# Optimization experiments

Hardware: AMD Instinct MI355X
Metric: run time of the kernel (lower is better)

The kernel has to match this reference:

```python
import jax, jax.numpy as jnp
from jax import lax
import numpy as np

VOCAB = 50000
EMBED = 300
UNITS = 512          # num_nodes[0]
D1 = 1024            # num_nodes[1]
D2 = 1024            # num_nodes[2]
NUM_CLASSES = 20
B, T = 64, 512


def setup_inputs() -> dict:
    key = jax.random.key(0)
    ks = jax.random.split(key, 12)
    s = 0.02
    return {
        "tokens": jax.random.randint(ks[0], (B, T), 0, VOCAB),
        "emb": jax.random.normal(ks[1], (VOCAB, EMBED), jnp.float32) * s,
        "Wx": jax.random.normal(ks[2], (EMBED, 4 * UNITS), jnp.float32) * s,
        "Wh": jax.random.normal(ks[3], (UNITS, 4 * UNITS), jnp.float32) * s,
        "b": jnp.zeros((4 * UNITS,), jnp.float32),
        "W1": jax.random.normal(ks[4], (UNITS, D1), jnp.float32) * s,
        "b1": jnp.zeros((D1,), jnp.float32),
        "W2": jax.random.normal(ks[5], (D1, D2), jnp.float32) * s,
        "b2": jnp.zeros((D2,), jnp.float32),
        "Wo": jax.random.normal(ks[6], (D2, NUM_CLASSES), jnp.float32) * s,
        "bo": jnp.zeros((NUM_CLASSES,), jnp.float32),
    }


def reference(tokens, emb, Wx, Wh, b, W1, b1, W2, b2, Wo, bo):
    # Embedding with mask_zero=True: token 0 timesteps are masked -> LSTM skips
    # the state update (Keras semantics).
    mask = (tokens != 0)                               # [B, T]
    x = emb[tokens]                                    # [B, T, E]
    units = Wh.shape[0]
    # Precompute input contribution to the gates (parallel over time).
    xg = jnp.einsum('bte,eg->btg', x, Wx) + b          # [B, T, 4U]

    def step(carry, inp):
        h, c = carry
        g_x, m = inp                                   # [B,4U], [B]
        g = g_x + h @ Wh                               # [B, 4U]
        i, f, cc, o = jnp.split(g, 4, axis=-1)         # Keras gate order i,f,c,o
        i = jax.nn.sigmoid(i)
        f = jax.nn.sigmoid(f)
        o = jax.nn.sigmoid(o)
        # activation='relu' replaces tanh in candidate and output transform.
        c_new = f * c + i * jax.nn.relu(cc)
        h_new = o * jax.nn.relu(c_new)
        m = m[:, None]
        h = jnp.where(m, h_new, h)
        c = jnp.where(m, c_new, c)
        return (h, c), None

    h0 = jnp.zeros((tokens.shape[0], units), x.dtype)
    (h, _), _ = lax.scan(step, (h0, h0),
                         (jnp.swapaxes(xg, 0, 1), mask.T))  # scan over T

    h = jax.nn.relu(h @ W1 + b1)
    h = jax.nn.relu(h @ W2 + b2)
    return jax.nn.softmax(h @ Wo + bo)
```

## Files before the change

### kernel.cpp

```cpp
#include <hip/hip_runtime.h>
#include <hip/hip_bf16.h>

#define B_   64
#define T_   512
#define E_   300
#define U_   512
#define G4_  2048
#define D1_  1024
#define D2_  1024
#define NC_  20
#define KP_  320

typedef __bf16 bf16x8 __attribute__((ext_vector_type(8)));
typedef float  f32x4  __attribute__((ext_vector_type(4)));

__device__ __forceinline__ float sigmoidf_(float x) { return 1.0f / (1.0f + __expf(-x)); }

__device__ __forceinline__ void gl_lds16(const void* g, void* l) {
    __builtin_amdgcn_global_load_lds(
        (const __attribute__((address_space(1))) unsigned int*)g,
        (__attribute__((address_space(3))) unsigned int*)l, 16, 0, 0);
}

__global__ void init_kernel(unsigned int* __restrict__ hz, int* __restrict__ flags) {
    int idx = blockIdx.x * 256 + threadIdx.x;
    if (idx < (B_ * U_ / 2)) hz[idx] = 0u;
    if (idx < 256) flags[idx] = 0;
}

__global__ __launch_bounds__(256) void prep_wxT(const float* __restrict__ Wx,
                                                __hip_bfloat16* __restrict__ wxT) {
    __shared__ __hip_bfloat16 t[64][65];
    const int n0 = blockIdx.x * 64;
    const int k0 = blockIdx.y * 64;
    const int tid = threadIdx.x;
    for (int i = tid; i < 4096; i += 256) {
        int r = i >> 6, c = i & 63;
        int k = k0 + r;
        float v = (k < E_) ? Wx[(size_t)k * G4_ + n0 + c] : 0.f;
        t[r][c] = __float2bfloat16(v);
    }
    __syncthreads();
    for (int i = tid; i < 4096; i += 256) {
        int r = i >> 6, c = i & 63;
        wxT[(size_t)(n0 + r) * KP_ + k0 + c] = t[c][r];
    }
}

__global__ __launch_bounds__(256) void prep_xb(const int* __restrict__ tokens,
                                               const float* __restrict__ emb,
                                               __hip_bfloat16* __restrict__ xb) {
    const int row = blockIdx.x * 4 + (threadIdx.x >> 6);
    const int ln  = threadIdx.x & 63;
    const int tok = tokens[row];
    const float* src = emb + (size_t)tok * E_;
    __hip_bfloat16* dst = xb + (size_t)row * KP_;
    for (int k = ln; k < KP_; k += 64)
        dst[k] = (k < E_) ? __float2bfloat16(src[k]) : __float2bfloat16(0.f);
}

__global__ __launch_bounds__(256) void xg_gemm(const __hip_bfloat16* __restrict__ xb,
                                               const __hip_bfloat16* __restrict__ wxT,
                                               const float* __restrict__ bias,
                                               __hip_bfloat16* __restrict__ xg) {
    const int n0g = blockIdx.x * 128;
    const int bt0 = blockIdx.y * 128;
    const int tid = threadIdx.x;
    const int w   = tid >> 6;
    const int ln  = tid & 63;
    const int fn  = ln & 15;
    const int quad = ln >> 4;
    const int m0  = (w >> 1) * 64;
    const int n0w = (w & 1) * 64;

    __shared__ __align__(16) __hip_bfloat16 As[128 * 32];
    __shared__ __align__(16) __hip_bfloat16 Bs[128 * 32];

    f32x4 acc[4][4];
    #pragma unroll
    for (int im = 0; im < 4; ++im)
        #pragma unroll
        for (int in = 0; in < 4; ++in)
            acc[im][in] = (f32x4){0.f, 0.f, 0.f, 0.f};

    const __hip_bfloat16* ga = xb  + (size_t)(bt0 + w * 32 + (ln >> 2)) * KP_ + (ln & 3) * 8;
    const __hip_bfloat16* gb = wxT + (size_t)(n0g + w * 32 + (ln >> 2)) * KP_ + (ln & 3) * 8;

    for (int kt = 0; kt < KP_ / 32; ++kt) {
        gl_lds16(ga,             &As[(w * 32) * 32]);
        gl_lds16(ga + 16 * KP_,  &As[(w * 32 + 16) * 32]);
        gl_lds16(gb,             &Bs[(w * 32) * 32]);
        gl_lds16(gb + 16 * KP_,  &Bs[(w * 32 + 16) * 32]);
        ga += 32; gb += 32;
        __syncthreads();

        bf16x8 af[4], bf[4];
        #pragma unroll
        for (int im = 0; im < 4; ++im)
            af[im] = *(const bf16x8*)&As[(m0 + im * 16 + fn) * 32 + quad * 8];
        #pragma unroll
        for (int in = 0; in < 4; ++in)
            bf[in] = *(const bf16x8*)&Bs[(n0w + in * 16 + fn) * 32 + quad * 8];
        #pragma unroll
        for (int im = 0; im < 4; ++im)
            #pragma unroll
            for (int in = 0; in < 4; ++in)
                acc[im][in] = __builtin_amdgcn_mfma_f32_16x16x32_bf16(
                    af[im], bf[in], acc[im][in], 0, 0, 0);
        __syncthreads();
    }

    #pragma unroll
    for (int in = 0; in < 4; ++in) {
        const int n = n0g + n0w + in * 16 + fn;
        const float bv = bias[n];
        #pragma unroll
        for (int im = 0; im < 4; ++im) {
            #pragma unroll
            for (int r = 0; r < 4; ++r) {
                int m = bt0 + m0 + im * 16 + quad * 4 + r;
                int bb = m >> 9, tt = m & 511;
                xg[(size_t)(tt * B_ + bb) * G4_ + n] =
                    __float2bfloat16(acc[im][in][r] + bv);
            }
        }
    }
}

__global__ __launch_bounds__(256) void lstm_kernel(const __hip_bfloat16* __restrict__ xg,
                                                   const int* __restrict__ tokens,
                                                   const float* __restrict__ Wh,
                                                   __hip_bfloat16* __restrict__ hbuf,
                                                   int* __restrict__ flags) {
    const int tid  = threadIdx.x;
    const int lane = tid & 63;
    const int wave = tid >> 6;
    const int x  = blockIdx.x & 7;
    const int r_ = blockIdx.x >> 3;
    const int ub = x * 4 + (r_ & 3);
    const int g  = r_ >> 2;
    const int u0 = ub * 16;

    __shared__ __align__(16) __hip_bfloat16 whsT[64][520];
    __shared__ __align__(16) __hip_bfloat16 hs[16][520];
    __shared__ float gbuf[16][64];
    __shared__ unsigned mask_lds[16][16];

    for (int idx = tid; idx < 64 * 512; idx += 256) {
        int c = idx & 63, k = idx >> 6;
        int col = ((c >> 4) << 9) + u0 + (c & 15);
        whsT[c][k] = __float2bfloat16(Wh[(size_t)k * G4_ + col]);
    }
    {
        int m = tid >> 4, wi = tid & 15;
        const int4* tp = (const int4*)(tokens + (size_t)(g * 16 + m) * T_ + wi * 32);
        unsigned bits = 0;
        #pragma unroll
        for (int q = 0; q < 8; ++q) {
            int4 v = tp[q];
            bits |= (v.x != 0 ? 1u : 0u) << (q * 4 + 0);
            bits |= (v.y != 0 ? 1u : 0u) << (q * 4 + 1);
            bits |= (v.z != 0 ? 1u : 0u) << (q * 4 + 2);
            bits |= (v.w != 0 ? 1u : 0u) << (q * 4 + 3);
        }
        mask_lds[m][wi] = bits;
    }

    float c0 = 0.f, c1 = 0.f, h0 = 0.f, h1 = 0.f;
    int* gflags = flags + g * 64;

    const int fn   = lane & 15;
    const int quad = lane >> 4;
    const int fc   = wave * 16 + fn;
    const int fcol = ((fc >> 4) << 9) + u0 + (fc & 15);

    __syncthreads();

    for (int s = 0; s < T_; ++s) {
        float xv[4];
        {
            #pragma unroll
            for (int r = 0; r < 4; ++r)
                xv[r] = __bfloat162float(
                    xg[(size_t)(s * B_ + g * 16 + quad * 4 + r) * G4_ + fcol]);
        }

        if (s > 0) {
            if (tid < 32) {
                while (__hip_atomic_load(&gflags[tid], __ATOMIC_RELAXED,
                                         __HIP_MEMORY_SCOPE_AGENT) < s)
                    __builtin_amdgcn_s_sleep(2);
            }
            __syncthreads();
        }

        {
            const uint4* hp = (const uint4*)(hbuf + (size_t)((s & 1) * B_ + g * 16) * U_);
            uint4 t0, t1, t2, t3;
            asm volatile(
                "global_load_dwordx4 %0, %4, off sc0 sc1\n\t"
                "global_load_dwordx4 %1, %5, off sc0 sc1\n\t"
                "global_load_dwordx4 %2, %6, off sc0 sc1\n\t"
                "s_waitcnt vmcnt(0)\n\t"
                "global_load_dwordx4 %3, %7, off sc0 sc1\n\t"
                "s_waitcnt vmcnt(0)"
                : "=&v"(t0), "=&v"(t1), "=&v"(t2), "=&v"(t3)
                : "v"(hp + tid), "v"(hp + tid + 256), "v"(hp + tid + 512),
                  "v"(hp + tid + 768)
                : "memory");
            int i0 = tid;        *((uint4*)&hs[i0 >> 6][(i0 & 63) * 8]) = t0;
            int i1 = tid + 256;  *((uint4*)&hs[i1 >> 6][(i1 & 63) * 8]) = t1;
            int i2 = tid + 512;  *((uint4*)&hs[i2 >> 6][(i2 & 63) * 8]) = t2;
            int i3 = tid + 768;  *((uint4*)&hs[i3 >> 6][(i3 & 63) * 8]) = t3;
        }
        __syncthreads();

        {
            f32x4 acc;
            #pragma unroll
            for (int r = 0; r < 4; ++r) acc[r] = xv[r];
            const __hip_bfloat16* arow = &hs[fn][quad * 8];
            const __hip_bfloat16* brow = &whsT[fc][quad * 8];
            #pragma unroll
            for (int kk = 0; kk < 16; ++kk) {
                bf16x8 av = *(const bf16x8*)(arow + kk * 32);
                bf16x8 bv = *(const bf16x8*)(brow + kk * 32);
                acc = __builtin_amdgcn_mfma_f32_16x16x32_bf16(av, bv, acc, 0, 0, 0);
            }
            #pragma unroll
            for (int r = 0; r < 4; ++r)
                gbuf[quad * 4 + r][fc] = acc[r];
        }
        __syncthreads();

        if (tid < 128) {
            const int m  = tid >> 3;
            const int u2 = (tid & 7) << 1;
            float gi0 = sigmoidf_(gbuf[m][u2]),       gi1 = sigmoidf_(gbuf[m][u2 + 1]);
            float gf0 = sigmoidf_(gbuf[m][16 + u2]),  gf1 = sigmoidf_(gbuf[m][17 + u2]);
            float gc0 = gbuf[m][32 + u2],             gc1 = gbuf[m][33 + u2];
            float go0 = sigmoidf_(gbuf[m][48 + u2]),  go1 = sigmoidf_(gbuf[m][49 + u2]);
            float cn0 = gf0 * c0 + gi0 * fmaxf(gc0, 0.f);
            float cn1 = gf1 * c1 + gi1 * fmaxf(gc1, 0.f);
            float hn0 = go0 * fmaxf(cn0, 0.f);
            float hn1 = go1 * fmaxf(cn1, 0.f);
            if ((mask_lds[m][s >> 5] >> (s & 31)) & 1u) {
                c0 = cn0; c1 = cn1; h0 = hn0; h1 = hn1;
            }
            __hip_bfloat162 hv;
            hv.x = __float2bfloat16(h0);
            hv.y = __float2bfloat16(h1);
            unsigned wv;
            __builtin_memcpy(&wv, &hv, 4);
            unsigned* dst = (unsigned*)hbuf +
                (((((s + 1) & 1) * B_ + g * 16 + m) * U_ + u0 + u2) >> 1);
            __hip_atomic_store(dst, wv, __ATOMIC_RELAXED, __HIP_MEMORY_SCOPE_AGENT);
        }
        __syncthreads();
        if (tid == 0)
            __hip_atomic_store(&gflags[ub], s + 1, __ATOMIC_RELAXED,
                               __HIP_MEMORY_SCOPE_AGENT);
    }
}

__global__ __launch_bounds__(256) void fc1_kernel(const __hip_bfloat16* __restrict__ h,
                                                  const float* __restrict__ W,
                                                  const float* __restrict__ bias,
                                                  float* __restrict__ y) {
    int b = blockIdx.x >> 2, ch = blockIdx.x & 3;
    __shared__ float xrow[U_];
    for (int i = threadIdx.x; i < U_; i += 256)
        xrow[i] = __bfloat162float(h[b * U_ + i]);
    __syncthreads();
    int n = ch * 256 + threadIdx.x;
    float acc = 0.f;
    #pragma unroll 4
    for (int k = 0; k < U_; ++k) acc = fmaf(xrow[k], W[(size_t)k * D1_ + n], acc);
    y[b * D1_ + n] = fmaxf(acc + bias[n], 0.f);
}

__global__ __launch_bounds__(256) void fc2_kernel(const float* __restrict__ x,
                                                  const float* __restrict__ W,
                                                  const float* __restrict__ bias,
                                                  float* __restrict__ y) {
    int b = blockIdx.x >> 2, ch = blockIdx.x & 3;
    __shared__ float xrow[D1_];
    for (int i = threadIdx.x; i < D1_; i += 256) xrow[i] = x[b * D1_ + i];
    __syncthreads();
    int n = ch * 256 + threadIdx.x;
    float acc = 0.f;
    #pragma unroll 4
    for (int k = 0; k < D1_; ++k) acc = fmaf(xrow[k], W[(size_t)k * D2_ + n], acc);
    y[b * D2_ + n] = fmaxf(acc + bias[n], 0.f);
}

__global__ __launch_bounds__(64) void out_kernel(const float* __restrict__ h2,
                                                 const float* __restrict__ Wo,
                                                 const float* __restrict__ bo,
                                                 float* __restrict__ out) {
    int b = blockIdx.x;
    __shared__ float xrow[D2_];
    __shared__ float lg[NC_];
    __shared__ float red[2];
    for (int i = threadIdx.x; i < D2_; i += 64) xrow[i] = h2[b * D2_ + i];
    __syncthreads();
    if (threadIdx.x < NC_) {
        float a = bo[threadIdx.x];
        for (int k = 0; k < D2_; ++k) a = fmaf(xrow[k], Wo[k * NC_ + threadIdx.x], a);
        lg[threadIdx.x] = a;
    }
    __syncthreads();
    if (threadIdx.x == 0) {
        float mx = lg[0];
        for (int c = 1; c < NC_; ++c) mx = fmaxf(mx, lg[c]);
        float sm = 0.f;
        for (int c = 0; c < NC_; ++c) sm += expf(lg[c] - mx);
        red[0] = mx; red[1] = 1.0f / sm;
    }
    __syncthreads();
    if (threadIdx.x < NC_)
        out[b * NC_ + threadIdx.x] = expf(lg[threadIdx.x] - red[0]) * red[1];
}

extern "C" void kernel_launch(void* const* d_in, const int* in_sizes, int n_in,
                              void* d_out, int out_size, void* d_ws, size_t ws_size,
                              hipStream_t stream) {
    const int*   tokens = (const int*)d_in[0];
    const float* emb    = (const float*)d_in[1];
    const float* Wx     = (const float*)d_in[2];
    const float* Wh     = (const float*)d_in[3];
    const float* b      = (const float*)d_in[4];
    const float* W1     = (const float*)d_in[5];
    const float* b1     = (const float*)d_in[6];
    const float* W2     = (const float*)d_in[7];
    const float* b2     = (const float*)d_in[8];
    const float* Wo     = (const float*)d_in[9];
    const float* bo     = (const float*)d_in[10];
    float* out = (float*)d_out;

    char* ws = (char*)d_ws;
    const size_t XG_BYTES   = (size_t)T_ * B_ * G4_ * 2;
    const size_t HBUF_BYTES = (size_t)2 * B_ * U_ * 2;
    __hip_bfloat16* xg   = (__hip_bfloat16*)ws;
    __hip_bfloat16* hbuf = (__hip_bfloat16*)(ws + XG_BYTES);
    int* flags           = (int*)(ws + XG_BYTES + HBUF_BYTES);
    char* p = ws + XG_BYTES + HBUF_BYTES + 1024;
    float* h1            = (float*)p;                 p += (size_t)B_ * D1_ * 4;
    float* h2            = (float*)p;                 p += (size_t)B_ * D2_ * 4;
    __hip_bfloat16* xb   = (__hip_bfloat16*)p;        p += (size_t)B_ * T_ * KP_ * 2;
    __hip_bfloat16* wxT  = (__hip_bfloat16*)p;

    init_kernel<<<64, 256, 0, stream>>>((unsigned int*)hbuf, flags);
    prep_wxT<<<dim3(32, 5), 256, 0, stream>>>(Wx, wxT);
    prep_xb<<<(B_ * T_) / 4, 256, 0, stream>>>(tokens, emb, xb);
    xg_gemm<<<dim3(16, 256), 256, 0, stream>>>(xb, wxT, b, xg);
    lstm_kernel<<<128, 256, 0, stream>>>(xg, tokens, Wh, hbuf, flags);
    fc1_kernel<<<256, 256, 0, stream>>>(hbuf, W1, b1, h1);
    fc2_kernel<<<256, 256, 0, stream>>>(h1, W2, b2, h2);
    out_kernel<<<64, 64, 0, stream>>>(h2, Wo, bo, out);
}
```

Baseline: 1.693 ms.

## Interleave two batch groups per LSTM block to overlap sync latency

Each LSTM block now handles two 16-row batch groups instead of one, halving the grid to 64 blocks. The step loop alternates between the groups, so the flag wait and hidden-state load for group B overlap with the gate compute for group A, hiding cross-block synchronisation latency. It also drops an intermediate s_waitcnt so all four hidden-state loads are issued together. In exchange each block does twice the MFMA and elementwise work per step serially and holds more LDS, and the group A flag is now published later in the step.

```diff
diff --git a/kernel.cpp b/kernel.cpp
--- a/kernel.cpp
+++ b/kernel.cpp
@@ -138,13 +138,15 @@
     const int x  = blockIdx.x & 7;
     const int r_ = blockIdx.x >> 3;
     const int ub = x * 4 + (r_ & 3);
-    const int g  = r_ >> 2;
+    const int p  = r_ >> 2;
+    const int gA = p * 2;
+    const int gB = p * 2 + 1;
     const int u0 = ub * 16;
 
     __shared__ __align__(16) __hip_bfloat16 whsT[64][520];
-    __shared__ __align__(16) __hip_bfloat16 hs[16][520];
-    __shared__ float gbuf[16][64];
-    __shared__ unsigned mask_lds[16][16];
+    __shared__ __align__(16) __hip_bfloat16 hs[2][16][520];
+    __shared__ float gbuf[2][16][64];
+    __shared__ unsigned mask_lds[2][16][16];
 
     for (int idx = tid; idx < 64 * 512; idx += 256) {
         int c = idx & 63, k = idx >> 6;
@@ -153,21 +155,27 @@
     }
     {
         int m = tid >> 4, wi = tid & 15;
-        const int4* tp = (const int4*)(tokens + (size_t)(g * 16 + m) * T_ + wi * 32);
-        unsigned bits = 0;
-        #pragma unroll
-        for (int q = 0; q < 8; ++q) {
-            int4 v = tp[q];
-            bits |= (v.x != 0 ? 1u : 0u) << (q * 4 + 0);
-            bits |= (v.y != 0 ? 1u : 0u) << (q * 4 + 1);
-            bits |= (v.z != 0 ? 1u : 0u) << (q * 4 + 2);
-            bits |= (v.w != 0 ? 1u : 0u) << (q * 4 + 3);
-        }
-        mask_lds[m][wi] = bits;
-    }
-
-    float c0 = 0.f, c1 = 0.f, h0 = 0.f, h1 = 0.f;
-    int* gflags = flags + g * 64;
+        #pragma unroll
+        for (int grp = 0; grp < 2; ++grp) {
+            const int4* tp = (const int4*)(tokens +
+                (size_t)((p * 2 + grp) * 16 + m) * T_ + wi * 32);
+            unsigned bits = 0;
+            #pragma unroll
+            for (int q = 0; q < 8; ++q) {
+                int4 v = tp[q];
+                bits |= (v.x != 0 ? 1u : 0u) << (q * 4 + 0);
+                bits |= (v.y != 0 ? 1u : 0u) << (q * 4 + 1);
+                bits |= (v.z != 0 ? 1u : 0u) << (q * 4 + 2);
+                bits |= (v.w != 0 ? 1u : 0u) << (q * 4 + 3);
+            }
+            mask_lds[grp][m][wi] = bits;
+        }
+    }
+
+    float cA0 = 0.f, cA1 = 0.f, hA0 = 0.f, hA1 = 0.f;
+    float cB0 = 0.f, cB1 = 0.f, hB0 = 0.f, hB1 = 0.f;
+    int* gfA = flags + gA * 64;
+    int* gfB = flags + gB * 64;
 
     const int fn   = lane & 15;
     const int quad = lane >> 4;
@@ -177,49 +185,47 @@
     __syncthreads();
 
     for (int s = 0; s < T_; ++s) {
-        float xv[4];
-        {
-            #pragma unroll
-            for (int r = 0; r < 4; ++r)
-                xv[r] = __bfloat162float(
-                    xg[(size_t)(s * B_ + g * 16 + quad * 4 + r) * G4_ + fcol]);
+        float xvA[4], xvB[4];
+        #pragma unroll
+        for (int r = 0; r < 4; ++r) {
+            xvA[r] = __bfloat162float(
+                xg[(size_t)(s * B_ + gA * 16 + quad * 4 + r) * G4_ + fcol]);
+            xvB[r] = __bfloat162float(
+                xg[(size_t)(s * B_ + gB * 16 + quad * 4 + r) * G4_ + fcol]);
         }
 
         if (s > 0) {
             if (tid < 32) {
-                while (__hip_atomic_load(&gflags[tid], __ATOMIC_RELAXED,
+                while (__hip_atomic_load(&gfA[tid], __ATOMIC_RELAXED,
                                          __HIP_MEMORY_SCOPE_AGENT) < s)
                     __builtin_amdgcn_s_sleep(2);
             }
             __syncthreads();
         }
-
         {
-            const uint4* hp = (const uint4*)(hbuf + (size_t)((s & 1) * B_ + g * 16) * U_);
+            const uint4* hp = (const uint4*)(hbuf + (size_t)((s & 1) * B_ + gA * 16) * U_);
             uint4 t0, t1, t2, t3;
             asm volatile(
                 "global_load_dwordx4 %0, %4, off sc0 sc1\n\t"
                 "global_load_dwordx4 %1, %5, off sc0 sc1\n\t"
                 "global_load_dwordx4 %2, %6, off sc0 sc1\n\t"
-                "s_waitcnt vmcnt(0)\n\t"
                 "global_load_dwordx4 %3, %7, off sc0 sc1\n\t"
                 "s_waitcnt vmcnt(0)"
                 : "=&v"(t0), "=&v"(t1), "=&v"(t2), "=&v"(t3)
                 : "v"(hp + tid), "v"(hp + tid + 256), "v"(hp + tid + 512),
                   "v"(hp + tid + 768)
                 : "memory");
-            int i0 = tid;        *((uint4*)&hs[i0 >> 6][(i0 & 63) * 8]) = t0;
-            int i1 = tid + 256;  *((uint4*)&hs[i1 >> 6][(i1 & 63) * 8]) = t1;
-            int i2 = tid + 512;  *((uint4*)&hs[i2 >> 6][(i2 & 63) * 8]) = t2;
-            int i3 = tid + 768;  *((uint4*)&hs[i3 >> 6][(i3 & 63) * 8]) = t3;
-        }
-        __syncthreads();
-
+            int i0 = tid;        *((uint4*)&hs[0][i0 >> 6][(i0 & 63) * 8]) = t0;
+            int i1 = tid + 256;  *((uint4*)&hs[0][i1 >> 6][(i1 & 63) * 8]) = t1;
+            int i2 = tid + 512;  *((uint4*)&hs[0][i2 >> 6][(i2 & 63) * 8]) = t2;
+            int i3 = tid + 768;  *((uint4*)&hs[0][i3 >> 6][(i3 & 63) * 8]) = t3;
+        }
+        __syncthreads();
         {
             f32x4 acc;
             #pragma unroll
-            for (int r = 0; r < 4; ++r) acc[r] = xv[r];
-            const __hip_bfloat16* arow = &hs[fn][quad * 8];
+            for (int r = 0; r < 4; ++r) acc[r] = xvA[r];
+            const __hip_bfloat16* arow = &hs[0][fn][quad * 8];
             const __hip_bfloat16* brow = &whsT[fc][quad * 8];
             #pragma unroll
             for (int kk = 0; kk < 16; ++kk) {
@@ -229,36 +235,106 @@
             }
             #pragma unroll
             for (int r = 0; r < 4; ++r)
-                gbuf[quad * 4 + r][fc] = acc[r];
-        }
-        __syncthreads();
-
+                gbuf[0][quad * 4 + r][fc] = acc[r];
+        }
+        __syncthreads();
         if (tid < 128) {
             const int m  = tid >> 3;
             const int u2 = (tid & 7) << 1;
-            float gi0 = sigmoidf_(gbuf[m][u2]),       gi1 = sigmoidf_(gbuf[m][u2 + 1]);
-            float gf0 = sigmoidf_(gbuf[m][16 + u2]),  gf1 = sigmoidf_(gbuf[m][17 + u2]);
-            float gc0 = gbuf[m][32 + u2],             gc1 = gbuf[m][33 + u2];
-            float go0 = sigmoidf_(gbuf[m][48 + u2]),  go1 = sigmoidf_(gbuf[m][49 + u2]);
-            float cn0 = gf0 * c0 + gi0 * fmaxf(gc0, 0.f);
-            float cn1 = gf1 * c1 + gi1 * fmaxf(gc1, 0.f);
+            float gi0 = sigmoidf_(gbuf[0][m][u2]),       gi1 = sigmoidf_(gbuf[0][m][u2 + 1]);
+            float gf0 = sigmoidf_(gbuf[0][m][16 + u2]),  gf1 = sigmoidf_(gbuf[0][m][17 + u2]);
+            float gc0 = gbuf[0][m][32 + u2],             gc1 = gbuf[0][m][33 + u2];
+            float go0 = sigmoidf_(gbuf[0][m][48 + u2]),  go1 = sigmoidf_(gbuf[0][m][49 + u2]);
+            float cn0 = gf0 * cA0 + gi0 * fmaxf(gc0, 0.f);
+            float cn1 = gf1 * cA1 + gi1 * fmaxf(gc1, 0.f);
             float hn0 = go0 * fmaxf(cn0, 0.f);
             float hn1 = go1 * fmaxf(cn1, 0.f);
-            if ((mask_lds[m][s >> 5] >> (s & 31)) & 1u) {
-                c0 = cn0; c1 = cn1; h0 = hn0; h1 = hn1;
+            if ((mask_lds[0][m][s >> 5] >> (s & 31)) & 1u) {
+                cA0 = cn0; cA1 = cn1; hA0 = hn0; hA1 = hn1;
             }
             __hip_bfloat162 hv;
-            hv.x = __float2bfloat16(h0);
-            hv.y = __float2bfloat16(h1);
+            hv.x = __float2bfloat16(hA0);
+            hv.y = __float2bfloat16(hA1);
             unsigned wv;
             __builtin_memcpy(&wv, &hv, 4);
             unsigned* dst = (unsigned*)hbuf +
-                (((((s + 1) & 1) * B_ + g * 16 + m) * U_ + u0 + u2) >> 1);
+                (((((s + 1) & 1) * B_ + gA * 16 + m) * U_ + u0 + u2) >> 1);
             __hip_atomic_store(dst, wv, __ATOMIC_RELAXED, __HIP_MEMORY_SCOPE_AGENT);
         }
+
+        if (s > 0) {
+            if (tid < 32) {
+                while (__hip_atomic_load(&gfB[tid], __ATOMIC_RELAXED,
+                                         __HIP_MEMORY_SCOPE_AGENT) < s)
+                    __builtin_amdgcn_s_sleep(2);
+            }
+        }
+        __syncthreads();
+        {
+            const uint4* hp = (const uint4*)(hbuf + (size_t)((s & 1) * B_ + gB * 16) * U_);
+            uint4 t0, t1, t2, t3;
+            asm volatile(
+                "global_load_dwordx4 %0, %4, off sc0 sc1\n\t"
+                "global_load_dwordx4 %1, %5, off sc0 sc1\n\t"
+                "global_load_dwordx4 %2, %6, off sc0 sc1\n\t"
+                "global_load_dwordx4 %3, %7, off sc0 sc1\n\t"
+                "s_waitcnt vmcnt(0)"
+                : "=&v"(t0), "=&v"(t1), "=&v"(t2), "=&v"(t3)
+                : "v"(hp + tid), "v"(hp + tid + 256), "v"(hp + tid + 512),
+                  "v"(hp + tid + 768)
+                : "memory");
+            int i0 = tid;        *((uint4*)&hs[1][i0 >> 6][(i0 & 63) * 8]) = t0;
+            int i1 = tid + 256;  *((uint4*)&hs[1][i1 >> 6][(i1 & 63) * 8]) = t1;
+            int i2 = tid + 512;  *((uint4*)&hs[1][i2 >> 6][(i2 & 63) * 8]) = t2;
+            int i3 = tid + 768;  *((uint4*)&hs[1][i3 >> 6][(i3 & 63) * 8]) = t3;
+        }
         __syncthreads();
         if (tid == 0)
-            __hip_atomic_store(&gflags[ub], s + 1, __ATOMIC_RELAXED,
+            __hip_atomic_store(&gfA[ub], s + 1, __ATOMIC_RELAXED,
+                               __HIP_MEMORY_SCOPE_AGENT);
+        {
+            f32x4 acc;
+            #pragma unroll
+            for (int r = 0; r < 4; ++r) acc[r] = xvB[r];
+            const __hip_bfloat16* arow = &hs[1][fn][quad * 8];
+            const __hip_bfloat16* brow = &whsT[fc][quad * 8];
+            #pragma unroll
+            for (int kk = 0; kk < 16; ++kk) {
+                bf16x8 av = *(const bf16x8*)(arow + kk * 32);
+                bf16x8 bv = *(const bf16x8*)(brow + kk * 32);
+                acc = __builtin_amdgcn_mfma_f32_16x16x32_bf16(av, bv, acc, 0, 0, 0);
+            }
+            #pragma unroll
+            for (int r = 0; r < 4; ++r)
+                gbuf[1][quad * 4 + r][fc] = acc[r];
+        }
+        __syncthreads();
+        if (tid < 128) {
+            const int m  = tid >> 3;
+            const int u2 = (tid & 7) << 1;
+            float gi0 = sigmoidf_(gbuf[1][m][u2]),       gi1 = sigmoidf_(gbuf[1][m][u2 + 1]);
+            float gf0 = sigmoidf_(gbuf[1][m][16 + u2]),  gf1 = sigmoidf_(gbuf[1][m][17 + u2]);
+            float gc0 = gbuf[1][m][32 + u2],             gc1 = gbuf[1][m][33 + u2];
+            float go0 = sigmoidf_(gbuf[1][m][48 + u2]),  go1 = sigmoidf_(gbuf[1][m][49 + u2]);
+            float cn0 = gf0 * cB0 + gi0 * fmaxf(gc0, 0.f);
+            float cn1 = gf1 * cB1 + gi1 * fmaxf(gc1, 0.f);
+            float hn0 = go0 * fmaxf(cn0, 0.f);
+            float hn1 = go1 * fmaxf(cn1, 0.f);
+            if ((mask_lds[1][m][s >> 5] >> (s & 31)) & 1u) {
+                cB0 = cn0; cB1 = cn1; hB0 = hn0; hB1 = hn1;
+            }
+            __hip_bfloat162 hv;
+            hv.x = __float2bfloat16(hB0);
+            hv.y = __float2bfloat16(hB1);
+            unsigned wv;
+            __builtin_memcpy(&wv, &hv, 4);
+            unsigned* dst = (unsigned*)hbuf +
+                (((((s + 1) & 1) * B_ + gB * 16 + m) * U_ + u0 + u2) >> 1);
+            __hip_atomic_store(dst, wv, __ATOMIC_RELAXED, __HIP_MEMORY_SCOPE_AGENT);
+        }
+        __syncthreads();
+        if (tid == 0)
+            __hip_atomic_store(&gfB[ub], s + 1, __ATOMIC_RELAXED,
                                __HIP_MEMORY_SCOPE_AGENT);
     }
 }
@@ -354,7 +430,7 @@
     prep_wxT<<<dim3(32, 5), 256, 0, stream>>>(Wx, wxT);
     prep_xb<<<(B_ * T_) / 4, 256, 0, stream>>>(tokens, emb, xb);
     xg_gemm<<<dim3(16, 256), 256, 0, stream>>>(xb, wxT, b, xg);
-    lstm_kernel<<<128, 256, 0, stream>>>(xg, tokens, Wh, hbuf, flags);
+    lstm_kernel<<<64, 256, 0, stream>>>(xg, tokens, Wh, hbuf, flags);
     fc1_kernel<<<256, 256, 0, stream>>>(hbuf, W1, b1, h1);
     fc2_kernel<<<256, 256, 0, stream>>>(h1, W2, b2, h2);
     out_kernel<<<64, 64, 0, stream>>>(h2, Wo, bo, out);
```

Result: slower. 2.362 ms (+39.6%).
